# Kernel optimization log

Hardware: AMD Instinct MI355X
Metric: run time of the kernel (lower is better)

Reference implementation:

```python
import jax, jax.numpy as jnp
import numpy as np

N, E, D, HGC, LG, NC = 20000, 320000, 256, 256, 4, 2
BN_EPS = 1e-5


def setup_inputs() -> dict:
    key = jax.random.key(0)
    ks = jax.random.split(key, 12)
    features = jax.random.normal(ks[0], (N, D), jnp.float32)
    edge_index = jax.random.randint(ks[1], (2, E), 0, N)
    edgenet_input = jax.random.uniform(ks[2], (E, 6), dtype=jnp.float32)
    edge_weight_override = jax.random.uniform(ks[3], (E,), dtype=jnp.float32)
    # ChebConv weights: K=3 weight matrices per layer; layer0 in=D==HGC so one stack works
    cheb_w = jax.random.normal(ks[4], (LG, 3, HGC, HGC), jnp.float32) * np.float32((2.0 / HGC) ** 0.5)
    w1 = jax.random.normal(ks[5], (LG * HGC, 256), jnp.float32) * np.float32((2.0 / (LG * HGC)) ** 0.5)
    b1 = jnp.zeros((256,), jnp.float32)
    bn_gamma = jnp.ones((256,), jnp.float32)
    bn_beta = jnp.zeros((256,), jnp.float32)
    bn_mean = jnp.zeros((256,), jnp.float32)
    bn_var = jnp.ones((256,), jnp.float32)
    w2 = jax.random.normal(ks[6], (256, NC), jnp.float32) * np.float32((2.0 / 256.0) ** 0.5)
    b2 = jnp.zeros((NC,), jnp.float32)
    return dict(features=features, edge_index=edge_index, edgenet_input=edgenet_input,
                edge_weight_override=edge_weight_override, cheb_w=cheb_w,
                w1=w1, b1=b1, bn_gamma=bn_gamma, bn_beta=bn_beta,
                bn_mean=bn_mean, bn_var=bn_var, w2=w2, b2=b2)


def reference(features, edge_index, edgenet_input, edge_weight_override, cheb_w,
              w1, b1, bn_gamma, bn_beta, bn_mean, bn_var, w2, b2):
    # eval mode: dropout / edge_dropout are no-ops; edge_weight_override bypasses PAE
    ew = edge_weight_override  # [E]
    row, col = edge_index[0], edge_index[1]  # source, target (PyG source_to_target)
    n = features.shape[0]
    # sym-normalized scaled Laplacian, lambda_max=2: L_hat = -D^{-1/2} A D^{-1/2} (diag 1-1=0)
    deg = jax.ops.segment_sum(ew, row, num_segments=n)
    dis = jnp.where(deg > 0, jax.lax.rsqrt(deg), 0.0)
    norm = -(dis[row] * ew * dis[col])  # [E]

    def prop(x):  # out[col] += norm * x[row]
        return jax.ops.segment_sum(norm[:, None] * x[row], col, num_segments=n)

    def cheb(x, W):  # W: [3, in, out]; Chebyshev recursion T0=x, T1=L_hat x, T2=2 L_hat T1 - T0
        tx0 = x
        tx1 = prop(x)
        out = tx0 @ W[0] + tx1 @ W[1]
        tx2 = 2.0 * prop(tx1) - tx0
        return out + tx2 @ W[2]

    h = jax.nn.relu(cheb(features, cheb_w[0]))
    jk = h
    for i in range(1, cheb_w.shape[0]):
        h = jax.nn.relu(cheb(h, cheb_w[i]))
        jk = jnp.concatenate((jk, h), axis=1)
    # classifier: Linear -> ReLU -> BatchNorm1d(eval) -> Linear
    z = jax.nn.relu(jk @ w1 + b1)
    z = (z - bn_mean) * (bn_gamma * jax.lax.rsqrt(bn_var + BN_EPS)) + bn_beta
    logit = z @ w2 + b2
    return logit, ew
```

## Files before the change

kernel.cpp:

```cpp
#include <hip/hip_runtime.h>
#include <hip/hip_bf16.h>

#define NN 20000
#define EE 320000
#define LGN 4

typedef unsigned short u16;
typedef short bf16x8 __attribute__((ext_vector_type(8)));
typedef float f32x4 __attribute__((ext_vector_type(4)));

__device__ __forceinline__ float bf2f(u16 v) {
    unsigned int u = ((unsigned int)v) << 16;
    float f; __builtin_memcpy(&f, &u, 4); return f;
}
__device__ __forceinline__ u16 f2bf(float f) {
    __hip_bfloat16 h = __float2bfloat16(f);
    u16 u; __builtin_memcpy(&u, &h, 2); return u;
}

__device__ __forceinline__ void gll16(const void* g, void* l) {
    __builtin_amdgcn_global_load_lds(
        (const __attribute__((address_space(1))) unsigned int*)g,
        (__attribute__((address_space(3))) unsigned int*)l, 16, 0, 0);
}

__global__ __launch_bounds__(256) void k_edge1(const int* __restrict__ ei,
                                               const float* __restrict__ ew,
                                               float* __restrict__ deg,
                                               int* __restrict__ counts,
                                               float* __restrict__ out_ew) {
    int e = blockIdx.x * 256 + threadIdx.x;
    if (e >= EE) return;
    int r = ei[e];
    float w = ew[e];
    atomicAdd(&deg[r], w);
    atomicAdd(&counts[ei[EE + e]], 1);
    out_ew[e] = w;
}

__global__ __launch_bounds__(256) void k_rsqrt(float* __restrict__ deg) {
    int i = blockIdx.x * 256 + threadIdx.x;
    if (i >= NN) return;
    float d = deg[i];
    deg[i] = (d > 0.f) ? rsqrtf(d) : 0.f;
}

__global__ __launch_bounds__(1024) void k_scan(const int* __restrict__ counts,
                                               int* __restrict__ offs) {
    __shared__ int part[1024];
    int t = threadIdx.x;
    const int C = (NN + 1023) / 1024;
    int lo = t * C, hi = min(lo + C, NN);
    int s = 0;
    for (int i = lo; i < hi; i++) s += counts[i];
    part[t] = s;
    __syncthreads();
    for (int off = 1; off < 1024; off <<= 1) {
        int add = (t >= off) ? part[t - off] : 0;
        __syncthreads();
        part[t] += add;
        __syncthreads();
    }
    int base = part[t] - s;
    for (int i = lo; i < hi; i++) { offs[i] = base; base += counts[i]; }
    if (t == 1023) offs[NN] = part[1023];
}

__global__ __launch_bounds__(256) void k_scatter(const int* __restrict__ ei,
                                                 const float* __restrict__ ew,
                                                 const float* __restrict__ dis,
                                                 const int* __restrict__ offs,
                                                 int* __restrict__ cursor,
                                                 int2* __restrict__ nbrs) {
    int e = blockIdx.x * 256 + threadIdx.x;
    if (e >= EE) return;
    int r = ei[e], c = ei[EE + e];
    float nm = -(dis[r] * ew[e] * dis[c]);
    int pidx = offs[c] + atomicAdd(&cursor[c], 1);
    nbrs[pidx] = make_int2(r, __float_as_int(nm));
}

__global__ __launch_bounds__(256) void k_cast(const float* __restrict__ src,
                                              u16* __restrict__ dst, int n) {
    int i = blockIdx.x * 256 + threadIdx.x;
    if (i < n) dst[i] = f2bf(src[i]);
}

__global__ __launch_bounds__(256) void k_castB(const float* __restrict__ src,
                                               u16* __restrict__ dst, int K) {
    int tid = blockIdx.x * 256 + threadIdx.x;
    if (tid >= (K >> 5) * 1024) return;
    int l = tid & 63, f = (tid >> 6) & 15, s = tid >> 10;
    int col = f * 16 + (l & 15);
    int kb = s * 32 + ((l >> 4) << 3);
    u16 tmp[8];
#pragma unroll
    for (int j = 0; j < 8; j++) tmp[j] = f2bf(src[(size_t)(kb + j) * 256 + col]);
    *(uint4*)(dst + (size_t)tid * 8) = *(uint4*)tmp;
}

__global__ __launch_bounds__(256) void k_foldbn(const float* __restrict__ g,
                                                const float* __restrict__ be,
                                                const float* __restrict__ mn,
                                                const float* __restrict__ vr,
                                                float* __restrict__ sc,
                                                float* __restrict__ sh) {
    int t = threadIdx.x;
    if (t < 256) {
        float s = g[t] * rsqrtf(vr[t] + 1e-5f);
        sc[t] = s;
        sh[t] = be[t] - mn[t] * s;
    }
}

__global__ __launch_bounds__(256) void k_prop(const u16* __restrict__ x, int ldx,
                                              const u16* __restrict__ xsub, int ldsub,
                                              int dotx2,
                                              u16* __restrict__ out, int ldo,
                                              const int* __restrict__ offs,
                                              const int2* __restrict__ nbrs) {
    int c = __builtin_amdgcn_readfirstlane(blockIdx.x * 4 + (threadIdx.x >> 6));
    int lane = threadIdx.x & 63;
    int s = offs[c], e = offs[c + 1];
    float a0 = 0.f, a1 = 0.f, a2 = 0.f, a3 = 0.f;
    for (int i = s; i < e; i += 16) {
        int2 mm[16];
        ushort4 xv[16];
#pragma unroll
        for (int j = 0; j < 8; j++) mm[j] = nbrs[i + j];
#pragma unroll
        for (int j = 0; j < 8; j++)
            xv[j] = *(const ushort4*)(x + (size_t)mm[j].x * ldx + lane * 4);
        bool more = (i + 8 < e);
        if (more) {
#pragma unroll
            for (int j = 8; j < 16; j++) mm[j] = nbrs[i + j];
#pragma unroll
            for (int j = 8; j < 16; j++)
                xv[j] = *(const ushort4*)(x + (size_t)mm[j].x * ldx + lane * 4);
        }
#pragma unroll
        for (int j = 0; j < 8; j++) {
            float w = (i + j < e) ? __int_as_float(mm[j].y) : 0.f;
            a0 += w * bf2f(xv[j].x);
            a1 += w * bf2f(xv[j].y);
            a2 += w * bf2f(xv[j].z);
            a3 += w * bf2f(xv[j].w);
        }
        if (more) {
#pragma unroll
            for (int j = 8; j < 16; j++) {
                float w = (i + j < e) ? __int_as_float(mm[j].y) : 0.f;
                a0 += w * bf2f(xv[j].x);
                a1 += w * bf2f(xv[j].y);
                a2 += w * bf2f(xv[j].z);
                a3 += w * bf2f(xv[j].w);
            }
        }
    }
    if (dotx2) {
        ushort4 xs = *(const ushort4*)(xsub + (size_t)c * ldsub + lane * 4);
        a0 = 2.f * a0 - bf2f(xs.x);
        a1 = 2.f * a1 - bf2f(xs.y);
        a2 = 2.f * a2 - bf2f(xs.z);
        a3 = 2.f * a3 - bf2f(xs.w);
    }
    ushort4 o;
    o.x = f2bf(a0); o.y = f2bf(a1); o.z = f2bf(a2); o.w = f2bf(a3);
    *(ushort4*)(out + (size_t)c * ldo + lane * 4) = o;
}

__global__ __launch_bounds__(256, 3) void k_gemm(
    const u16* __restrict__ A0, const u16* __restrict__ A1,
    const u16* __restrict__ A2, const u16* __restrict__ A3,
    int lda0, int lda1, int lda2, int lda3,
    int K, const u16* __restrict__ Bf,
    int mode,
    u16* __restrict__ outb, int ldob,
    const float* __restrict__ bias, const float* __restrict__ sc,
    const float* __restrict__ sh,
    const float* __restrict__ w2, const float* __restrict__ b2,
    float* __restrict__ outlog) {
    __shared__ __align__(16) u16 lds[18432];
    int t = threadIdx.x;
    int wv = t >> 6, l = t & 63;
    int q = l >> 4, l16 = l & 15;
    int m0 = blockIdx.x * 64;
    int n0 = wv * 64;
    const int steps = K >> 5;

    f32x4 acc[4][4] = {};

    int arow = min(m0 + wv * 16 + l16, NN - 1);

    auto stageA = [&](int buf, int s) {
        int kt = s * 32;
        int ch = kt >> 8;
        const u16* ap;
        int la;
        if (ch == 0) { ap = A0; la = lda0; }
        else if (ch == 1) { ap = A1; la = lda1; }
        else if (ch == 2) { ap = A2; la = lda2; }
        else { ap = A3; la = lda3; }
        gll16(ap + (size_t)arow * la + (kt & 255) + q * 8, lds + buf * 2048 + wv * 512);
    };

    const u16* bfw = Bf + (size_t)(wv * 4) * 512 + l * 8;
    auto loadB = [&](bf16x8* dst, int s) {
#pragma unroll
        for (int j = 0; j < 4; j++)
            dst[j] = *(const bf16x8*)(bfw + (size_t)s * 8192 + j * 512);
    };
    auto comp = [&](int buf, const bf16x8* b) {
        const u16* base = lds + buf * 2048;
        bf16x8 a[4];
#pragma unroll
        for (int mh = 0; mh < 4; mh++)
            a[mh] = *(const bf16x8*)(base + mh * 512 + l * 8);
#pragma unroll
        for (int mh = 0; mh < 4; mh++)
#pragma unroll
            for (int j = 0; j < 4; j++)
                acc[mh][j] =
                    __builtin_amdgcn_mfma_f32_16x16x32_bf16(a[mh], b[j], acc[mh][j], 0, 0, 0);
    };

    bf16x8 bA[4], bB[4];
    loadB(bA, 0);
    stageA(0, 0);
    stageA(1, 1);
    stageA(2, 2);
    for (int s = 0; s < steps; s += 2) {
        if (s == 0)               asm volatile("s_waitcnt vmcnt(2)" ::: "memory");
        else if (s == steps - 2)  asm volatile("s_waitcnt vmcnt(9)" ::: "memory");
        else                      asm volatile("s_waitcnt vmcnt(10)" ::: "memory");
        __builtin_amdgcn_s_barrier();
        __builtin_amdgcn_sched_barrier(0);
        loadB(bB, s + 1);
        __builtin_amdgcn_sched_barrier(0);
        if (s + 3 < steps) stageA((s + 3) & 3, s + 3);
        __builtin_amdgcn_sched_barrier(0);
        comp(s & 3, bA);
        if (s == 0)               asm volatile("s_waitcnt vmcnt(6)" ::: "memory");
        else if (s == steps - 2)  asm volatile("s_waitcnt vmcnt(8)" ::: "memory");
        else                      asm volatile("s_waitcnt vmcnt(10)" ::: "memory");
        __builtin_amdgcn_s_barrier();
        __builtin_amdgcn_sched_barrier(0);
        if (s + 2 < steps) loadB(bA, s + 2);
        __builtin_amdgcn_sched_barrier(0);
        if (s + 4 < steps) stageA((s + 4) & 3, s + 4);
        __builtin_amdgcn_sched_barrier(0);
        comp((s + 1) & 3, bB);
    }
    __syncthreads();

    if (mode == 0) {
        u16* Cs = lds + wv * 4608;
#pragma unroll
        for (int mh = 0; mh < 4; mh++)
#pragma unroll
            for (int j = 0; j < 4; j++)
#pragma unroll
                for (int i = 0; i < 4; i++) {
                    float v = acc[mh][j][i];
                    v = v > 0.f ? v : 0.f;
                    Cs[(mh * 16 + q * 4 + i) * 72 + j * 16 + l16] = f2bf(v);
                }
#pragma unroll
        for (int j = 0; j < 8; j++) {
            int f = j * 64 + l;
            int r = f >> 3, cc = (f & 7) * 8;
            uint4 cv = *(const uint4*)&Cs[r * 72 + cc];
            int row = m0 + r;
            if (row < NN) *(uint4*)(outb + (size_t)row * ldob + n0 + cc) = cv;
        }
    } else {
        float bi[4], s4[4], h4[4], wa[4], wb[4];
#pragma unroll
        for (int j = 0; j < 4; j++) {
            int col = n0 + j * 16 + l16;
            bi[j] = bias[col];
            s4[j] = sc[col];
            h4[j] = sh[col];
            wa[j] = w2[2 * col];
            wb[j] = w2[2 * col + 1];
        }
        float* red = (float*)lds;
#pragma unroll
        for (int mh = 0; mh < 4; mh++)
#pragma unroll
            for (int i = 0; i < 4; i++) {
                float p0 = 0.f, p1 = 0.f;
#pragma unroll
                for (int j = 0; j < 4; j++) {
                    float v = acc[mh][j][i] + bi[j];
                    v = v > 0.f ? v : 0.f;
                    v = v * s4[j] + h4[j];
                    p0 += v * wa[j];
                    p1 += v * wb[j];
                }
#pragma unroll
                for (int off = 1; off < 16; off <<= 1) {
                    p0 += __shfl_xor(p0, off, 64);
                    p1 += __shfl_xor(p1, off, 64);
                }
                if (l16 == 0) {
                    int rl = mh * 16 + q * 4 + i;
                    red[(wv * 64 + rl) * 2 + 0] = p0;
                    red[(wv * 64 + rl) * 2 + 1] = p1;
                }
            }
        __syncthreads();
        if (t < 128) {
            int rl = t >> 1, cp = t & 1;
            float v = red[(0 * 64 + rl) * 2 + cp] + red[(1 * 64 + rl) * 2 + cp] +
                      red[(2 * 64 + rl) * 2 + cp] + red[(3 * 64 + rl) * 2 + cp];
            int row = m0 + rl;
            if (row < NN) outlog[(size_t)row * 2 + cp] = v + b2[cp];
        }
    }
}

extern "C" void kernel_launch(void* const* d_in, const int* in_sizes, int n_in,
                              void* d_out, int out_size, void* d_ws, size_t ws_size,
                              hipStream_t stream) {
    const float* features = (const float*)d_in[0];
    const int* ei = (const int*)d_in[1];
    const float* ew = (const float*)d_in[3];
    const float* cheb_w = (const float*)d_in[4];
    const float* w1 = (const float*)d_in[5];
    const float* b1 = (const float*)d_in[6];
    const float* g = (const float*)d_in[7];
    const float* be = (const float*)d_in[8];
    const float* mn = (const float*)d_in[9];
    const float* vr = (const float*)d_in[10];
    const float* w2 = (const float*)d_in[11];
    const float* b2 = (const float*)d_in[12];
    float* out = (float*)d_out;

    char* p = (char*)d_ws;
    auto alloc = [&](size_t bytes) -> char* {
        char* r = p;
        p += (bytes + 255) & ~(size_t)255;
        return r;
    };
    float* deg = (float*)alloc((size_t)NN * 4);
    int* counts = (int*)alloc((size_t)(NN + 1) * 4);
    int* cursor = (int*)alloc((size_t)NN * 4);
    size_t zero_bytes = (size_t)(p - (char*)deg);
    int* offs = (int*)alloc((size_t)(NN + 1) * 4);
    int2* nbrs = (int2*)alloc((size_t)(EE + 16) * 8);
    u16* xb = (u16*)alloc((size_t)NN * 256 * 2);
    u16* tx1 = (u16*)alloc((size_t)NN * 256 * 2);
    u16* tx2 = (u16*)alloc((size_t)NN * 256 * 2);
    u16* jk = (u16*)alloc((size_t)NN * 1024 * 2);
    u16* chebT = (u16*)alloc((size_t)LGN * 3 * 256 * 256 * 2);
    u16* w1T = (u16*)alloc((size_t)1024 * 256 * 2);
    float* sc = (float*)alloc(256 * 4);
    float* sh = (float*)alloc(256 * 4);

    hipMemsetAsync(deg, 0, zero_bytes, stream);
    hipMemsetAsync(nbrs + EE, 0, 16 * sizeof(int2), stream);
    k_edge1<<<(EE + 255) / 256, 256, 0, stream>>>(ei, ew, deg, counts, out + (size_t)NN * 2);
    k_rsqrt<<<(NN + 255) / 256, 256, 0, stream>>>(deg);
    k_scan<<<1, 1024, 0, stream>>>(counts, offs);
    k_scatter<<<(EE + 255) / 256, 256, 0, stream>>>(ei, ew, deg, offs, cursor, nbrs);
    k_cast<<<((NN * 256) + 255) / 256, 256, 0, stream>>>(features, xb, NN * 256);
    for (int i = 0; i < LGN; i++)
        k_castB<<<96, 256, 0, stream>>>(cheb_w + (size_t)i * 768 * 256,
                                        chebT + (size_t)i * 256 * 768, 768);
    k_castB<<<128, 256, 0, stream>>>(w1, w1T, 1024);
    k_foldbn<<<1, 256, 0, stream>>>(g, be, mn, vr, sc, sh);

    const int gg = (NN + 63) / 64;
    for (int i = 0; i < LGN; i++) {
        const u16* x = (i == 0) ? xb : (jk + (size_t)(i - 1) * 256);
        int ldx = (i == 0) ? 256 : 1024;
        k_prop<<<NN / 4, 256, 0, stream>>>(x, ldx, (const u16*)nullptr, 0, 0, tx1, 256, offs,
                                           nbrs);
        k_prop<<<NN / 4, 256, 0, stream>>>(tx1, 256, x, ldx, 1, tx2, 256, offs, nbrs);
        k_gemm<<<gg, 256, 0, stream>>>(
            x, tx1, tx2, (const u16*)nullptr, ldx, 256, 256, 0, 768,
            chebT + (size_t)i * 256 * 768, 0, jk + (size_t)i * 256, 1024, (const float*)nullptr,
            (const float*)nullptr, (const float*)nullptr, (const float*)nullptr,
            (const float*)nullptr, (float*)nullptr);
    }
    k_gemm<<<gg, 256, 0, stream>>>(jk, jk + 256, jk + 512, jk + 768, 1024, 1024, 1024, 1024,
                                   1024, w1T, 1, (u16*)nullptr, 0, b1, sc, sh, w2, b2, out);
}
```

Measured before the change: 458.7 us.

## Restructure SpMM prop to split columns across blocks and edges across lane groups

The propagation kernel now gives each wave a 64-column slice of a node, with 8 lane groups each handling a different neighbor and 8 lanes loading 16-byte vectors, followed by an xor-shuffle reduction across groups. The grid grows fourfold so each block covers one column slice of 4 nodes. The aim is more memory parallelism per wave on the gather and fewer serialized per-edge steps. Separately, the rsqrt kernel is folded into the scatter kernel, and the four per-layer weight casts are merged into one launch with a 2D grid. In exchange, each neighbor row is fetched as 4 separate 128-byte pieces by different blocks, and the shuffle reduction adds work.

```diff
diff --git a/kernel.cpp b/kernel.cpp
--- a/kernel.cpp
+++ b/kernel.cpp
@@ -7,6 +7,7 @@
 
 typedef unsigned short u16;
 typedef short bf16x8 __attribute__((ext_vector_type(8)));
+typedef unsigned short u16x8 __attribute__((ext_vector_type(8)));
 typedef float f32x4 __attribute__((ext_vector_type(4)));
 
 __device__ __forceinline__ float bf2f(u16 v) {
@@ -36,13 +37,6 @@
     atomicAdd(&deg[r], w);
     atomicAdd(&counts[ei[EE + e]], 1);
     out_ew[e] = w;
-}
-
-__global__ __launch_bounds__(256) void k_rsqrt(float* __restrict__ deg) {
-    int i = blockIdx.x * 256 + threadIdx.x;
-    if (i >= NN) return;
-    float d = deg[i];
-    deg[i] = (d > 0.f) ? rsqrtf(d) : 0.f;
 }
 
 __global__ __launch_bounds__(1024) void k_scan(const int* __restrict__ counts,
@@ -68,14 +62,17 @@
 
 __global__ __launch_bounds__(256) void k_scatter(const int* __restrict__ ei,
                                                  const float* __restrict__ ew,
-                                                 const float* __restrict__ dis,
+                                                 const float* __restrict__ deg,
                                                  const int* __restrict__ offs,
                                                  int* __restrict__ cursor,
                                                  int2* __restrict__ nbrs) {
     int e = blockIdx.x * 256 + threadIdx.x;
     if (e >= EE) return;
     int r = ei[e], c = ei[EE + e];
-    float nm = -(dis[r] * ew[e] * dis[c]);
+    float dr = deg[r], dc = deg[c];
+    float ir = (dr > 0.f) ? rsqrtf(dr) : 0.f;
+    float ic = (dc > 0.f) ? rsqrtf(dc) : 0.f;
+    float nm = -(ir * ew[e] * ic);
     int pidx = offs[c] + atomicAdd(&cursor[c], 1);
     nbrs[pidx] = make_int2(r, __float_as_int(nm));
 }
@@ -88,6 +85,8 @@
 
 __global__ __launch_bounds__(256) void k_castB(const float* __restrict__ src,
                                                u16* __restrict__ dst, int K) {
+    src += (size_t)blockIdx.y * K * 256;
+    dst += (size_t)blockIdx.y * K * 256;
     int tid = blockIdx.x * 256 + threadIdx.x;
     if (tid >= (K >> 5) * 1024) return;
     int l = tid & 63, f = (tid >> 6) & 15, s = tid >> 10;
@@ -119,55 +118,71 @@
                                               u16* __restrict__ out, int ldo,
                                               const int* __restrict__ offs,
                                               const int2* __restrict__ nbrs) {
-    int c = __builtin_amdgcn_readfirstlane(blockIdx.x * 4 + (threadIdx.x >> 6));
-    int lane = threadIdx.x & 63;
+    int sl = blockIdx.x & 3;
+    int c = __builtin_amdgcn_readfirstlane((blockIdx.x >> 2) * 4 + (threadIdx.x >> 6));
+    int l = threadIdx.x & 63;
+    int g = l >> 3;
+    int o = l & 7;
+    int cb = sl * 64 + o * 8;
     int s = offs[c], e = offs[c + 1];
     float a0 = 0.f, a1 = 0.f, a2 = 0.f, a3 = 0.f;
+    float a4 = 0.f, a5 = 0.f, a6 = 0.f, a7 = 0.f;
     for (int i = s; i < e; i += 16) {
-        int2 mm[16];
-        ushort4 xv[16];
-#pragma unroll
-        for (int j = 0; j < 8; j++) mm[j] = nbrs[i + j];
-#pragma unroll
-        for (int j = 0; j < 8; j++)
-            xv[j] = *(const ushort4*)(x + (size_t)mm[j].x * ldx + lane * 4);
+        int2 m0 = nbrs[i + g];
+        int2 m1 = nbrs[i + 8 + g];
+        u16x8 x0 = *(const u16x8*)(x + (size_t)m0.x * ldx + cb);
         bool more = (i + 8 < e);
+        u16x8 x1 = x0;
+        if (more) x1 = *(const u16x8*)(x + (size_t)m1.x * ldx + cb);
+        float w0 = (i + g < e) ? __int_as_float(m0.y) : 0.f;
+        a0 += w0 * bf2f(x0[0]);
+        a1 += w0 * bf2f(x0[1]);
+        a2 += w0 * bf2f(x0[2]);
+        a3 += w0 * bf2f(x0[3]);
+        a4 += w0 * bf2f(x0[4]);
+        a5 += w0 * bf2f(x0[5]);
+        a6 += w0 * bf2f(x0[6]);
+        a7 += w0 * bf2f(x0[7]);
         if (more) {
-#pragma unroll
-            for (int j = 8; j < 16; j++) mm[j] = nbrs[i + j];
-#pragma unroll
-            for (int j = 8; j < 16; j++)
-                xv[j] = *(const ushort4*)(x + (size_t)mm[j].x * ldx + lane * 4);
+            float w1 = (i + 8 + g < e) ? __int_as_float(m1.y) : 0.f;
+            a0 += w1 * bf2f(x1[0]);
+            a1 += w1 * bf2f(x1[1]);
+            a2 += w1 * bf2f(x1[2]);
+            a3 += w1 * bf2f(x1[3]);
+            a4 += w1 * bf2f(x1[4]);
+            a5 += w1 * bf2f(x1[5]);
+            a6 += w1 * bf2f(x1[6]);
+            a7 += w1 * bf2f(x1[7]);
         }
-#pragma unroll
-        for (int j = 0; j < 8; j++) {
-            float w = (i + j < e) ? __int_as_float(mm[j].y) : 0.f;
-            a0 += w * bf2f(xv[j].x);
-            a1 += w * bf2f(xv[j].y);
-            a2 += w * bf2f(xv[j].z);
-            a3 += w * bf2f(xv[j].w);
-        }
-        if (more) {
-#pragma unroll
-            for (int j = 8; j < 16; j++) {
-                float w = (i + j < e) ? __int_as_float(mm[j].y) : 0.f;
-                a0 += w * bf2f(xv[j].x);
-                a1 += w * bf2f(xv[j].y);
-                a2 += w * bf2f(xv[j].z);
-                a3 += w * bf2f(xv[j].w);
-            }
-        }
+    }
+#pragma unroll
+    for (int off = 8; off < 64; off <<= 1) {
+        a0 += __shfl_xor(a0, off, 64);
+        a1 += __shfl_xor(a1, off, 64);
+        a2 += __shfl_xor(a2, off, 64);
+        a3 += __shfl_xor(a3, off, 64);
+        a4 += __shfl_xor(a4, off, 64);
+        a5 += __shfl_xor(a5, off, 64);
+        a6 += __shfl_xor(a6, off, 64);
+        a7 += __shfl_xor(a7, off, 64);
     }
     if (dotx2) {
-        ushort4 xs = *(const ushort4*)(xsub + (size_t)c * ldsub + lane * 4);
-        a0 = 2.f * a0 - bf2f(xs.x);
-        a1 = 2.f * a1 - bf2f(xs.y);
-        a2 = 2.f * a2 - bf2f(xs.z);
-        a3 = 2.f * a3 - bf2f(xs.w);
-    }
-    ushort4 o;
-    o.x = f2bf(a0); o.y = f2bf(a1); o.z = f2bf(a2); o.w = f2bf(a3);
-    *(ushort4*)(out + (size_t)c * ldo + lane * 4) = o;
+        u16x8 xs = *(const u16x8*)(xsub + (size_t)c * ldsub + cb);
+        a0 = 2.f * a0 - bf2f(xs[0]);
+        a1 = 2.f * a1 - bf2f(xs[1]);
+        a2 = 2.f * a2 - bf2f(xs[2]);
+        a3 = 2.f * a3 - bf2f(xs[3]);
+        a4 = 2.f * a4 - bf2f(xs[4]);
+        a5 = 2.f * a5 - bf2f(xs[5]);
+        a6 = 2.f * a6 - bf2f(xs[6]);
+        a7 = 2.f * a7 - bf2f(xs[7]);
+    }
+    if (g == 0) {
+        u16 ov[8];
+        ov[0] = f2bf(a0); ov[1] = f2bf(a1); ov[2] = f2bf(a2); ov[3] = f2bf(a3);
+        ov[4] = f2bf(a4); ov[5] = f2bf(a5); ov[6] = f2bf(a6); ov[7] = f2bf(a7);
+        *(uint4*)(out + (size_t)c * ldo + cb) = *(uint4*)ov;
+    }
 }
 
 __global__ __launch_bounds__(256, 3) void k_gemm(
@@ -362,23 +377,21 @@
     hipMemsetAsync(deg, 0, zero_bytes, stream);
     hipMemsetAsync(nbrs + EE, 0, 16 * sizeof(int2), stream);
     k_edge1<<<(EE + 255) / 256, 256, 0, stream>>>(ei, ew, deg, counts, out + (size_t)NN * 2);
-    k_rsqrt<<<(NN + 255) / 256, 256, 0, stream>>>(deg);
     k_scan<<<1, 1024, 0, stream>>>(counts, offs);
     k_scatter<<<(EE + 255) / 256, 256, 0, stream>>>(ei, ew, deg, offs, cursor, nbrs);
     k_cast<<<((NN * 256) + 255) / 256, 256, 0, stream>>>(features, xb, NN * 256);
-    for (int i = 0; i < LGN; i++)
-        k_castB<<<96, 256, 0, stream>>>(cheb_w + (size_t)i * 768 * 256,
-                                        chebT + (size_t)i * 256 * 768, 768);
-    k_castB<<<128, 256, 0, stream>>>(w1, w1T, 1024);
+    k_castB<<<dim3(96, LGN), 256, 0, stream>>>(cheb_w, chebT, 768);
+    k_castB<<<dim3(128, 1), 256, 0, stream>>>(w1, w1T, 1024);
     k_foldbn<<<1, 256, 0, stream>>>(g, be, mn, vr, sc, sh);
 
     const int gg = (NN + 63) / 64;
+    const int pg = (NN / 4) * 4;
     for (int i = 0; i < LGN; i++) {
         const u16* x = (i == 0) ? xb : (jk + (size_t)(i - 1) * 256);
         int ldx = (i == 0) ? 256 : 1024;
-        k_prop<<<NN / 4, 256, 0, stream>>>(x, ldx, (const u16*)nullptr, 0, 0, tx1, 256, offs,
-                                           nbrs);
-        k_prop<<<NN / 4, 256, 0, stream>>>(tx1, 256, x, ldx, 1, tx2, 256, offs, nbrs);
+        k_prop<<<pg, 256, 0, stream>>>(x, ldx, (const u16*)nullptr, 0, 0, tx1, 256, offs,
+                                       nbrs);
+        k_prop<<<pg, 256, 0, stream>>>(tx1, 256, x, ldx, 1, tx2, 256, offs, nbrs);
         k_gemm<<<gg, 256, 0, stream>>>(
             x, tx1, tx2, (const u16*)nullptr, ldx, 256, 256, 0, 768,
             chebT + (size_t)i * 256 * 768, 0, jk + (size_t)i * 256, 1024, (const float*)nullptr,
```

After: 528.4 us. 1.15x slower.
